# Optimization experiments

Hardware: AMD Instinct MI355X
Metric: run time of the kernel (lower is better)

Reference implementation:

```python
import jax, jax.numpy as jnp
import numpy as np

EPS = 1e-6  # EPS[torch.float32]
B, N = 4096, 64
MAX_ITER = 5


def setup_inputs() -> dict:
    key = jax.random.key(0)
    x = jax.random.normal(key, (B, N, N), dtype=jnp.float32)
    # SPD input, as assumed by the matrix-log layer (EEG covariance-like)
    M = x @ jnp.swapaxes(x, -1, -2) / N + 1e-3 * jnp.eye(N, dtype=jnp.float32)
    return {"input": M}


def _qr_algorithm(A, max_iter=MAX_ITER):
    # 5 iterations of the batched QR eigen-iteration, as in the torch source
    n = A.shape[-1]
    eye = jnp.broadcast_to(jnp.eye(n, dtype=A.dtype), A.shape)

    def body(carry, _):
        A_k, Q_total = carry
        Q, R = jnp.linalg.qr(A_k)
        return (R @ Q, Q_total @ Q), None

    (A_k, Q_total), _ = jax.lax.scan(body, (A, eye), None, length=max_iter)
    s = jnp.diagonal(A_k, axis1=-2, axis2=-1)  # approx eigenvalues [B, n]
    return s, Q_total  # Q_total: approx eigenvectors [B, n, n]


def reference(input):
    s, U = _qr_algorithm(input)
    smod = jnp.log(jnp.clip(s, EPS))  # sym_logm.value: clamp then log
    # U @ diag(smod) @ U^T, without materializing diag_embed
    X = (U * smod[..., None, :]) @ jnp.swapaxes(U, -1, -2)
    return X
```

## Files before the change

kernel.cpp:

```cpp
#include <hip/hip_runtime.h>
#include <math.h>

#define N 64
#define MAX_ITER 5

__device__ __forceinline__ float rl(float x, int lane) {
    return __uint_as_float(__builtin_amdgcn_readlane(__float_as_uint(x), lane));
}

__global__ __launch_bounds__(64)
__attribute__((amdgpu_waves_per_eu(1, 2)))
void logm_kernel(const float* __restrict__ gin, float* __restrict__ gout) {
    __shared__ __align__(16) float G[N * N];
    const int t = threadIdx.x;
    const long b = blockIdx.x;
    const float* __restrict__ in = gin + b * (long)(N * N);
    float* __restrict__ out = gout + b * (long)(N * N);

    float a[N], r[N], qt[N];

    #pragma unroll
    for (int i = 0; i < N; ++i) a[i] = in[i * N + t];
    #pragma unroll
    for (int i = 0; i < N; ++i) qt[i] = (i == t) ? 1.0f : 0.0f;

    float betaS = 0.f, v0S = 0.f, alS = 0.f;

    for (int iter = 0; iter < MAX_ITER; ++iter) {
        float dotA, dotQ, wA, wQ;
        {
            float dA0 = 0.f, dA1 = 0.f, dQ0 = 0.f, dQ1 = 0.f;
            #pragma unroll
            for (int i = 0; i < N; ++i) {
                const float c = rl(a[i], 0);
                if (i & 1) { dA1 = fmaf(c, a[i], dA1); dQ1 = fmaf(c, qt[i], dQ1); }
                else       { dA0 = fmaf(c, a[i], dA0); dQ0 = fmaf(c, qt[i], dQ0); }
            }
            dotA = dA0 + dA1; dotQ = dQ0 + dQ1;
            wA = a[0]; wQ = qt[0];
        }

        #pragma unroll
        for (int kb = 0; kb < 8; ++kb) {
            const int dkEnd = (kb == 7) ? 7 : 8;
            for (int dk = 0; dk < dkEnd; ++dk) {
                const int k = 8 * kb + dk;
                const int k1 = k + 1;
                const float ss = rl(dotA, k);
                const float x0 = rl(wA, k);
                const float nrm = sqrtf(ss);
                const float alpha = (x0 >= 0.f) ? -nrm : nrm;
                const float v0 = x0 - alpha;
                const float vtv = fmaf(v0, v0, ss - x0 * x0);
                const float beta = (vtv > 1e-30f) ? __fdividef(2.0f, vtv) : 0.f;
                const float ca = beta * fmaf(-alpha, wA, dotA);
                const float cq = beta * fmaf(-alpha, wQ, dotQ);
                const float caE = (t > k) ? ca : 0.f;
                betaS = (t == k) ? beta  : betaS;
                v0S   = (t == k) ? v0    : v0S;
                alS   = (t == k) ? alpha : alS;

                float nA0 = 0.f, nA1 = 0.f, nQ0 = 0.f, nQ1 = 0.f, nwA = 0.f, nwQ = 0.f;
                #pragma unroll
                for (int i0 = 8 * kb; i0 < N; i0 += 8) {
                    #pragma unroll
                    for (int u = 0; u < 8; ++u) {
                        const int i = i0 + u;
                        float cu = rl(a[i], k);
                        if (i0 == 8 * kb) cu = (i > k) ? cu : ((i == k) ? v0 : 0.f);
                        a[i]  = fmaf(-caE, cu, a[i]);
                        qt[i] = fmaf(-cq,  cu, qt[i]);
                        float c2 = rl(a[i], k1);
                        if (i0 == 8 * kb) c2 = (i > k) ? c2 : 0.f;
                        if (u & 1) { nA1 = fmaf(c2, a[i], nA1); nQ1 = fmaf(c2, qt[i], nQ1); }
                        else       { nA0 = fmaf(c2, a[i], nA0); nQ0 = fmaf(c2, qt[i], nQ0); }
                        if ((i0 == 8 * kb && u > 0) || (kb < 7 && i0 == 8 * kb + 8 && u == 0)) {
                            const bool e = (i == k1);
                            nwA = e ? a[i]  : nwA;
                            nwQ = e ? qt[i] : nwQ;
                        }
                    }
                }
                dotA = nA0 + nA1; dotQ = nQ0 + nQ1; wA = nwA; wQ = nwQ;
            }
        }

        const float diagR = (t == N - 1) ? a[N - 1] : alS;
        #pragma unroll
        for (int j = 0; j < N; j += 4) {
            float4 w; w.x = a[j]; w.y = a[j + 1]; w.z = a[j + 2]; w.w = a[j + 3];
            *reinterpret_cast<float4*>(&G[(t << 6) + ((j + (t << 2)) & 63)]) = w;
        }
        G[(t << 6) + ((5 * t) & 63)] = v0S;

        float dR;
        {
            #pragma unroll
            for (int j = 0; j < N; ++j) {
                const float g = G[(j << 6) + ((t + (j << 2)) & 63)];
                r[j] = (j > t) ? g : ((j == t) ? diagR : 0.f);
            }
            float d0 = 0.f, d1 = 0.f;
            #pragma unroll
            for (int j = 0; j < N; j += 4) {
                const float4 v = *reinterpret_cast<const float4*>(&G[j]);
                d0 = fmaf(v.x, r[j],     d0);
                d1 = fmaf(v.y, r[j + 1], d1);
                d0 = fmaf(v.z, r[j + 2], d0);
                d1 = fmaf(v.w, r[j + 3], d1);
            }
            dR = d0 + d1;
        }

        for (int k = 0; k < N - 1; ++k) {
            const int k1 = k + 1;
            const float cc = rl(betaS, k) * dR;
            float nD0 = 0.f, nD1 = 0.f;
            #pragma unroll
            for (int j0 = 0; j0 < N; j0 += 8) {
                if (j0 + 8 > k) {
                    #pragma unroll
                    for (int h = 0; h < 2; ++h) {
                        const int jc = j0 + 4 * h;
                        float4 vk  = *reinterpret_cast<const float4*>(
                            &G[(k  << 6) + ((jc + (k  << 2)) & 63)]);
                        float4 vk1 = *reinterpret_cast<const float4*>(
                            &G[(k1 << 6) + ((jc + (k1 << 2)) & 63)]);
                        if (jc <= k) {
                            vk.x  = (jc + 0 >= k)  ? vk.x  : 0.f;
                            vk.y  = (jc + 1 >= k)  ? vk.y  : 0.f;
                            vk.z  = (jc + 2 >= k)  ? vk.z  : 0.f;
                            vk.w  = (jc + 3 >= k)  ? vk.w  : 0.f;
                            vk1.x = (jc + 0 >= k1) ? vk1.x : 0.f;
                            vk1.y = (jc + 1 >= k1) ? vk1.y : 0.f;
                            vk1.z = (jc + 2 >= k1) ? vk1.z : 0.f;
                            vk1.w = (jc + 3 >= k1) ? vk1.w : 0.f;
                        }
                        r[jc + 0] = fmaf(-cc, vk.x, r[jc + 0]); nD0 = fmaf(vk1.x, r[jc + 0], nD0);
                        r[jc + 1] = fmaf(-cc, vk.y, r[jc + 1]); nD1 = fmaf(vk1.y, r[jc + 1], nD1);
                        r[jc + 2] = fmaf(-cc, vk.z, r[jc + 2]); nD0 = fmaf(vk1.z, r[jc + 2], nD0);
                        r[jc + 3] = fmaf(-cc, vk.w, r[jc + 3]); nD1 = fmaf(vk1.w, r[jc + 3], nD1);
                    }
                }
            }
            dR = nD0 + nD1;
        }
        #pragma unroll
        for (int j = 0; j < N; ++j) a[j] = r[j];
    }

    #pragma unroll
    for (int l = 0; l < N; ++l) {
        const float dl = rl(a[l], l);
        const float sml = __logf(fmaxf(dl, 1e-6f));
        a[l] = sml * qt[l];
    }
    #pragma unroll
    for (int l = 0; l < N; l += 4) {
        float4 w; w.x = qt[l]; w.y = qt[l + 1]; w.z = qt[l + 2]; w.w = qt[l + 3];
        *reinterpret_cast<float4*>(&G[(t << 6) + ((l + (t << 2)) & 63)]) = w;
    }
    #pragma unroll 2
    for (int j = 0; j < N; ++j) {
        float e0 = 0.f, e1 = 0.f, e2 = 0.f, e3 = 0.f;
        #pragma unroll
        for (int l = 0; l < N; l += 4) {
            const float4 u4 = *reinterpret_cast<const float4*>(
                &G[(j << 6) + ((l + (j << 2)) & 63)]);
            e0 = fmaf(a[l + 0], u4.x, e0);
            e1 = fmaf(a[l + 1], u4.y, e1);
            e2 = fmaf(a[l + 2], u4.z, e2);
            e3 = fmaf(a[l + 3], u4.w, e3);
        }
        out[j * N + t] = (e0 + e1) + (e2 + e3);
    }
}

extern "C" void kernel_launch(void* const* d_in, const int* in_sizes, int n_in,
                              void* d_out, int out_size, void* d_ws, size_t ws_size,
                              hipStream_t stream) {
    const float* in = (const float*)d_in[0];
    float* out = (float*)d_out;
    const int batch = in_sizes[0] / (N * N);
    hipLaunchKernelGGL(logm_kernel, dim3(batch), dim3(64), 0, stream, in, out);
}
```

Before: 1.355 ms.

## Split QR and Q-accumulation across two waves per block

Measured after the change: 3.663 ms. 2.7x slower.

```diff
diff --git a/kernel.cpp b/kernel.cpp
--- a/kernel.cpp
+++ b/kernel.cpp
@@ -8,160 +8,175 @@
     return __uint_as_float(__builtin_amdgcn_readlane(__float_as_uint(x), lane));
 }
 
-__global__ __launch_bounds__(64)
-__attribute__((amdgpu_waves_per_eu(1, 2)))
+__global__ __launch_bounds__(128)
 void logm_kernel(const float* __restrict__ gin, float* __restrict__ gout) {
     __shared__ __align__(16) float G[N * N];
-    const int t = threadIdx.x;
+    __shared__ float P[N];
+    const int t = threadIdx.x & 63;
+    const bool isQR = threadIdx.x < 64;
     const long b = blockIdx.x;
     const float* __restrict__ in = gin + b * (long)(N * N);
     float* __restrict__ out = gout + b * (long)(N * N);
 
-    float a[N], r[N], qt[N];
-
-    #pragma unroll
-    for (int i = 0; i < N; ++i) a[i] = in[i * N + t];
-    #pragma unroll
-    for (int i = 0; i < N; ++i) qt[i] = (i == t) ? 1.0f : 0.0f;
-
-    float betaS = 0.f, v0S = 0.f, alS = 0.f;
+    float a[N];
+    if (isQR) {
+        #pragma unroll
+        for (int i = 0; i < N; ++i) a[i] = in[i * N + t];
+    } else {
+        #pragma unroll
+        for (int i = 0; i < N; ++i) a[i] = (i == t) ? 1.0f : 0.0f;
+    }
+
+    float betaS = 0.f, v0S = 0.f, alS = 0.f, diagR = 0.f;
 
     for (int iter = 0; iter < MAX_ITER; ++iter) {
-        float dotA, dotQ, wA, wQ;
-        {
-            float dA0 = 0.f, dA1 = 0.f, dQ0 = 0.f, dQ1 = 0.f;
+        if (isQR) {
+            float dotA, wA;
+            {
+                float dA0 = 0.f, dA1 = 0.f;
+                #pragma unroll
+                for (int i = 0; i < N; ++i) {
+                    const float c = rl(a[i], 0);
+                    if (i & 1) dA1 = fmaf(c, a[i], dA1);
+                    else       dA0 = fmaf(c, a[i], dA0);
+                }
+                dotA = dA0 + dA1; wA = a[0];
+            }
             #pragma unroll
-            for (int i = 0; i < N; ++i) {
-                const float c = rl(a[i], 0);
-                if (i & 1) { dA1 = fmaf(c, a[i], dA1); dQ1 = fmaf(c, qt[i], dQ1); }
-                else       { dA0 = fmaf(c, a[i], dA0); dQ0 = fmaf(c, qt[i], dQ0); }
-            }
-            dotA = dA0 + dA1; dotQ = dQ0 + dQ1;
-            wA = a[0]; wQ = qt[0];
-        }
-
-        #pragma unroll
-        for (int kb = 0; kb < 8; ++kb) {
-            const int dkEnd = (kb == 7) ? 7 : 8;
-            for (int dk = 0; dk < dkEnd; ++dk) {
-                const int k = 8 * kb + dk;
-                const int k1 = k + 1;
-                const float ss = rl(dotA, k);
-                const float x0 = rl(wA, k);
-                const float nrm = sqrtf(ss);
-                const float alpha = (x0 >= 0.f) ? -nrm : nrm;
-                const float v0 = x0 - alpha;
-                const float vtv = fmaf(v0, v0, ss - x0 * x0);
-                const float beta = (vtv > 1e-30f) ? __fdividef(2.0f, vtv) : 0.f;
-                const float ca = beta * fmaf(-alpha, wA, dotA);
-                const float cq = beta * fmaf(-alpha, wQ, dotQ);
-                const float caE = (t > k) ? ca : 0.f;
-                betaS = (t == k) ? beta  : betaS;
-                v0S   = (t == k) ? v0    : v0S;
-                alS   = (t == k) ? alpha : alS;
-
-                float nA0 = 0.f, nA1 = 0.f, nQ0 = 0.f, nQ1 = 0.f, nwA = 0.f, nwQ = 0.f;
-                #pragma unroll
-                for (int i0 = 8 * kb; i0 < N; i0 += 8) {
+            for (int kb = 0; kb < 8; ++kb) {
+                const int dkEnd = (kb == 7) ? 7 : 8;
+                for (int dk = 0; dk < dkEnd; ++dk) {
+                    const int k = 8 * kb + dk;
+                    const int k1 = k + 1;
+                    const float ss = rl(dotA, k);
+                    const float x0 = rl(wA, k);
+                    const float nrm = sqrtf(ss);
+                    const float alpha = (x0 >= 0.f) ? -nrm : nrm;
+                    const float v0 = x0 - alpha;
+                    const float vtv = fmaf(v0, v0, ss - x0 * x0);
+                    const float beta = (vtv > 1e-30f) ? __fdividef(2.0f, vtv) : 0.f;
+                    const float ca = beta * fmaf(-alpha, wA, dotA);
+                    const float caE = (t > k) ? ca : 0.f;
+                    betaS = (t == k) ? beta  : betaS;
+                    v0S   = (t == k) ? v0    : v0S;
+                    alS   = (t == k) ? alpha : alS;
+
+                    float nA0 = 0.f, nA1 = 0.f, nwA = 0.f;
                     #pragma unroll
-                    for (int u = 0; u < 8; ++u) {
-                        const int i = i0 + u;
-                        float cu = rl(a[i], k);
-                        if (i0 == 8 * kb) cu = (i > k) ? cu : ((i == k) ? v0 : 0.f);
-                        a[i]  = fmaf(-caE, cu, a[i]);
-                        qt[i] = fmaf(-cq,  cu, qt[i]);
-                        float c2 = rl(a[i], k1);
-                        if (i0 == 8 * kb) c2 = (i > k) ? c2 : 0.f;
-                        if (u & 1) { nA1 = fmaf(c2, a[i], nA1); nQ1 = fmaf(c2, qt[i], nQ1); }
-                        else       { nA0 = fmaf(c2, a[i], nA0); nQ0 = fmaf(c2, qt[i], nQ0); }
-                        if ((i0 == 8 * kb && u > 0) || (kb < 7 && i0 == 8 * kb + 8 && u == 0)) {
-                            const bool e = (i == k1);
-                            nwA = e ? a[i]  : nwA;
-                            nwQ = e ? qt[i] : nwQ;
+                    for (int i0 = 8 * kb; i0 < N; i0 += 8) {
+                        #pragma unroll
+                        for (int u = 0; u < 8; ++u) {
+                            const int i = i0 + u;
+                            float cu = rl(a[i], k);
+                            if (i0 == 8 * kb) cu = (i > k) ? cu : ((i == k) ? v0 : 0.f);
+                            a[i] = fmaf(-caE, cu, a[i]);
+                            float c2 = rl(a[i], k1);
+                            if (i0 == 8 * kb) c2 = (i > k) ? c2 : 0.f;
+                            if (u & 1) nA1 = fmaf(c2, a[i], nA1);
+                            else       nA0 = fmaf(c2, a[i], nA0);
+                            if ((i0 == 8 * kb && u > 0) || (kb < 7 && i0 == 8 * kb + 8 && u == 0)) {
+                                nwA = (i == k1) ? a[i] : nwA;
+                            }
                         }
                     }
-                }
-                dotA = nA0 + nA1; dotQ = nQ0 + nQ1; wA = nwA; wQ = nwQ;
-            }
-        }
-
-        const float diagR = (t == N - 1) ? a[N - 1] : alS;
-        #pragma unroll
-        for (int j = 0; j < N; j += 4) {
-            float4 w; w.x = a[j]; w.y = a[j + 1]; w.z = a[j + 2]; w.w = a[j + 3];
-            *reinterpret_cast<float4*>(&G[(t << 6) + ((j + (t << 2)) & 63)]) = w;
-        }
-        G[(t << 6) + ((5 * t) & 63)] = v0S;
-
-        float dR;
-        {
-            #pragma unroll
-            for (int j = 0; j < N; ++j) {
-                const float g = G[(j << 6) + ((t + (j << 2)) & 63)];
-                r[j] = (j > t) ? g : ((j == t) ? diagR : 0.f);
-            }
-            float d0 = 0.f, d1 = 0.f;
+                    dotA = nA0 + nA1; wA = nwA;
+                }
+            }
+            diagR = (t == N - 1) ? a[N - 1] : alS;
             #pragma unroll
             for (int j = 0; j < N; j += 4) {
-                const float4 v = *reinterpret_cast<const float4*>(&G[j]);
-                d0 = fmaf(v.x, r[j],     d0);
-                d1 = fmaf(v.y, r[j + 1], d1);
-                d0 = fmaf(v.z, r[j + 2], d0);
-                d1 = fmaf(v.w, r[j + 3], d1);
-            }
-            dR = d0 + d1;
-        }
-
-        for (int k = 0; k < N - 1; ++k) {
-            const int k1 = k + 1;
-            const float cc = rl(betaS, k) * dR;
-            float nD0 = 0.f, nD1 = 0.f;
-            #pragma unroll
-            for (int j0 = 0; j0 < N; j0 += 8) {
-                if (j0 + 8 > k) {
-                    #pragma unroll
-                    for (int h = 0; h < 2; ++h) {
-                        const int jc = j0 + 4 * h;
-                        float4 vk  = *reinterpret_cast<const float4*>(
-                            &G[(k  << 6) + ((jc + (k  << 2)) & 63)]);
-                        float4 vk1 = *reinterpret_cast<const float4*>(
-                            &G[(k1 << 6) + ((jc + (k1 << 2)) & 63)]);
-                        if (jc <= k) {
-                            vk.x  = (jc + 0 >= k)  ? vk.x  : 0.f;
-                            vk.y  = (jc + 1 >= k)  ? vk.y  : 0.f;
-                            vk.z  = (jc + 2 >= k)  ? vk.z  : 0.f;
-                            vk.w  = (jc + 3 >= k)  ? vk.w  : 0.f;
-                            vk1.x = (jc + 0 >= k1) ? vk1.x : 0.f;
-                            vk1.y = (jc + 1 >= k1) ? vk1.y : 0.f;
-                            vk1.z = (jc + 2 >= k1) ? vk1.z : 0.f;
-                            vk1.w = (jc + 3 >= k1) ? vk1.w : 0.f;
+                float4 w; w.x = a[j]; w.y = a[j + 1]; w.z = a[j + 2]; w.w = a[j + 3];
+                *reinterpret_cast<float4*>(&G[(t << 6) + ((j + (t << 2)) & 63)]) = w;
+            }
+            G[(t << 6) + ((5 * t) & 63)] = v0S;
+            P[t] = betaS;
+        }
+        __syncthreads();
+
+        {
+            const float bq = P[t];
+            if (isQR) {
+                #pragma unroll
+                for (int j = 0; j < N; ++j) {
+                    const float g = G[(j << 6) + ((t + (j << 2)) & 63)];
+                    a[j] = (j > t) ? g : ((j == t) ? diagR : 0.f);
+                }
+            }
+            float dd;
+            {
+                float d0 = 0.f, d1 = 0.f;
+                #pragma unroll
+                for (int j = 0; j < N; j += 4) {
+                    const float4 v = *reinterpret_cast<const float4*>(&G[j]);
+                    d0 = fmaf(v.x, a[j],     d0);
+                    d1 = fmaf(v.y, a[j + 1], d1);
+                    d0 = fmaf(v.z, a[j + 2], d0);
+                    d1 = fmaf(v.w, a[j + 3], d1);
+                }
+                dd = d0 + d1;
+            }
+            for (int k = 0; k < N - 1; ++k) {
+                const int k1 = k + 1;
+                const float cc = rl(bq, k) * dd;
+                float nD0 = 0.f, nD1 = 0.f;
+                #pragma unroll
+                for (int j0 = 0; j0 < N; j0 += 8) {
+                    if (j0 + 8 > k) {
+                        #pragma unroll
+                        for (int h = 0; h < 2; ++h) {
+                            const int jc = j0 + 4 * h;
+                            float4 vk  = *reinterpret_cast<const float4*>(
+                                &G[(k  << 6) + ((jc + (k  << 2)) & 63)]);
+                            float4 vk1 = *reinterpret_cast<const float4*>(
+                                &G[(k1 << 6) + ((jc + (k1 << 2)) & 63)]);
+                            if (jc <= k) {
+                                vk.x  = (jc + 0 >= k)  ? vk.x  : 0.f;
+                                vk.y  = (jc + 1 >= k)  ? vk.y  : 0.f;
+                                vk.z  = (jc + 2 >= k)  ? vk.z  : 0.f;
+                                vk.w  = (jc + 3 >= k)  ? vk.w  : 0.f;
+                                vk1.x = (jc + 0 >= k1) ? vk1.x : 0.f;
+                                vk1.y = (jc + 1 >= k1) ? vk1.y : 0.f;
+                                vk1.z = (jc + 2 >= k1) ? vk1.z : 0.f;
+                                vk1.w = (jc + 3 >= k1) ? vk1.w : 0.f;
+                            }
+                            a[jc + 0] = fmaf(-cc, vk.x, a[jc + 0]); nD0 = fmaf(vk1.x, a[jc + 0], nD0);
+                            a[jc + 1] = fmaf(-cc, vk.y, a[jc + 1]); nD1 = fmaf(vk1.y, a[jc + 1], nD1);
+                            a[jc + 2] = fmaf(-cc, vk.z, a[jc + 2]); nD0 = fmaf(vk1.z, a[jc + 2], nD0);
+                            a[jc + 3] = fmaf(-cc, vk.w, a[jc + 3]); nD1 = fmaf(vk1.w, a[jc + 3], nD1);
                         }
-                        r[jc + 0] = fmaf(-cc, vk.x, r[jc + 0]); nD0 = fmaf(vk1.x, r[jc + 0], nD0);
-                        r[jc + 1] = fmaf(-cc, vk.y, r[jc + 1]); nD1 = fmaf(vk1.y, r[jc + 1], nD1);
-                        r[jc + 2] = fmaf(-cc, vk.z, r[jc + 2]); nD0 = fmaf(vk1.z, r[jc + 2], nD0);
-                        r[jc + 3] = fmaf(-cc, vk.w, r[jc + 3]); nD1 = fmaf(vk1.w, r[jc + 3], nD1);
                     }
                 }
-            }
-            dR = nD0 + nD1;
-        }
-        #pragma unroll
-        for (int j = 0; j < N; ++j) a[j] = r[j];
-    }
-
+                dd = nD0 + nD1;
+            }
+        }
+        __syncthreads();
+    }
+
+    if (isQR) {
+        P[t] = __logf(fmaxf(a[t], 1e-6f));
+    } else {
+        #pragma unroll
+        for (int l = 0; l < N; l += 4) {
+            float4 w; w.x = a[l]; w.y = a[l + 1]; w.z = a[l + 2]; w.w = a[l + 3];
+            *reinterpret_cast<float4*>(&G[(t << 6) + ((l + (t << 2)) & 63)]) = w;
+        }
+    }
+    __syncthreads();
+    const float sv = P[t];
+    if (isQR) {
+        #pragma unroll
+        for (int l = 0; l < N; l += 4) {
+            const float4 u = *reinterpret_cast<const float4*>(
+                &G[(t << 6) + ((l + (t << 2)) & 63)]);
+            a[l] = u.x; a[l + 1] = u.y; a[l + 2] = u.z; a[l + 3] = u.w;
+        }
+    }
     #pragma unroll
-    for (int l = 0; l < N; ++l) {
-        const float dl = rl(a[l], l);
-        const float sml = __logf(fmaxf(dl, 1e-6f));
-        a[l] = sml * qt[l];
-    }
-    #pragma unroll
-    for (int l = 0; l < N; l += 4) {
-        float4 w; w.x = qt[l]; w.y = qt[l + 1]; w.z = qt[l + 2]; w.w = qt[l + 3];
-        *reinterpret_cast<float4*>(&G[(t << 6) + ((l + (t << 2)) & 63)]) = w;
-    }
+    for (int l = 0; l < N; ++l) a[l] = rl(sv, l) * a[l];
+    const int jbase = isQR ? 0 : 32;
     #pragma unroll 2
-    for (int j = 0; j < N; ++j) {
+    for (int jj = 0; jj < 32; ++jj) {
+        const int j = jbase + jj;
         float e0 = 0.f, e1 = 0.f, e2 = 0.f, e3 = 0.f;
         #pragma unroll
         for (int l = 0; l < N; l += 4) {
@@ -182,5 +197,5 @@
     const float* in = (const float*)d_in[0];
     float* out = (float*)d_out;
     const int batch = in_sizes[0] / (N * N);
-    hipLaunchKernelGGL(logm_kernel, dim3(batch), dim3(64), 0, stream, in, out);
+    hipLaunchKernelGGL(logm_kernel, dim3(batch), dim3(128), 0, stream, in, out);
 }
```
